# Kernel tuning notes

Hardware: AMD Instinct MI355X
Metric: run time of the kernel (lower is better)

## Reference

```python
import jax, jax.numpy as jnp
import numpy as np

B, N, M, C = 32, 4096, 512, 256  # batch, grid points, retained modes, latent channels


def setup_inputs() -> dict:
    key = jax.random.key(0)
    k1, k2 = jax.random.split(key)
    v = jax.random.normal(k1, (B, N, C), dtype=jnp.float32)
    # glorot-style scale for a (C, C) per-mode transform: std = 1/sqrt(C)
    transform_R = jax.random.normal(k2, (M, C, C), dtype=jnp.float32) * np.float32(1.0 / np.sqrt(C))
    return {"v": v, "transform_R": transform_R}


def reference(v, transform_R):
    # v: (B, N, C) real; transform_R: (M, C, C) real, applied to complex modes
    n = v.shape[1]
    m = transform_R.shape[0]
    f = jnp.fft.rfft(v, axis=1)                     # (B, N//2+1, C) complex64
    fm = f[:, :m]                                   # keep low-frequency modes (B, M, C)
    # per-mode channel mixing: out[b,m,o] = sum_i R[m,i,o] * f[b,m,i]
    gm = jnp.einsum('mio,bmi->bmo', transform_R.astype(fm.dtype), fm)
    g = jnp.zeros_like(f).at[:, :m].set(gm)         # zero-pad high modes back
    return v + jnp.fft.irfft(g, n=n, axis=1)        # residual add, (B, N, C)
```

## Files before the change

### kernel.cpp

```cpp
#include <hip/hip_runtime.h>
#include <hip/hip_fp16.h>
#include <math.h>


constexpr int BB = 32;
constexpr int CC = 256;
constexpr int MM = 512;

constexpr float PI2_4096 = 1.5339807878856412e-3f;
constexpr float PI2_512  = 1.2271846303085130e-2f;
constexpr float PI2_64   = 9.8174770424681035e-2f;
constexpr float PI_4     = 0.78539816339744831f;

typedef _Float16 f16x8 __attribute__((ext_vector_type(8)));
typedef float f32x4 __attribute__((ext_vector_type(4)));

__device__ __forceinline__ float2 cadd(float2 a, float2 b){ return make_float2(a.x+b.x, a.y+b.y); }
__device__ __forceinline__ float2 csub(float2 a, float2 b){ return make_float2(a.x-b.x, a.y-b.y); }
__device__ __forceinline__ float2 cmulf(float2 a, float2 b){ return make_float2(a.x*b.x - a.y*b.y, a.x*b.y + a.y*b.x); }

template<int S>
__device__ __forceinline__ void dif8(float2 x[8]) {
    const float R = 0.70710678118654752f;
    const float Sf = (float)S;
    float2 a0=cadd(x[0],x[4]), a1=cadd(x[1],x[5]), a2=cadd(x[2],x[6]), a3=cadd(x[3],x[7]);
    float2 d0=csub(x[0],x[4]), d1=csub(x[1],x[5]), d2=csub(x[2],x[6]), d3=csub(x[3],x[7]);
    float2 t5 = cmulf(d1, make_float2(R, -R*Sf));
    float2 t6 = make_float2(Sf*d2.y, -Sf*d2.x);
    float2 t7 = cmulf(d3, make_float2(-R, -R*Sf));
    float2 b0=cadd(a0,a2), b1=cadd(a1,a3), b2=csub(a0,a2), e3=csub(a1,a3);
    float2 b3=make_float2(Sf*e3.y, -Sf*e3.x);
    float2 b4=cadd(d0,t6), b5=cadd(t5,t7), b6=csub(d0,t6), e7=csub(t5,t7);
    float2 b7=make_float2(Sf*e7.y, -Sf*e7.x);
    x[0]=cadd(b0,b1); x[4]=csub(b0,b1);
    x[2]=cadd(b2,b3); x[6]=csub(b2,b3);
    x[1]=cadd(b4,b5); x[5]=csub(b4,b5);
    x[3]=cadd(b6,b7); x[7]=csub(b6,b7);
}

__device__ __forceinline__ void twid7(float2 x[8], float ang) {
    float s, c;
    __sincosf(ang, &s, &c);
    float2 w = make_float2(c, s), cur = w;
    x[1] = cmulf(x[1], cur);
    #pragma unroll
    for (int k = 2; k < 8; ++k) { cur = cmulf(cur, w); x[k] = cmulf(x[k], cur); }
}

__global__ __launch_bounds__(256) void k1a_kernel(const float* __restrict__ v,
                                                  __half2* __restrict__ ybuf, int b0) {
    __shared__ float2 T[64 * 33];
    const int blk = blockIdx.x;
    const int ct = blk & 1;
    const int n2 = (blk >> 1) & 63;
    const int bl = blk >> 7;
    const int bat = b0 + bl;
    const int t = threadIdx.x;
    const int p = t & 63;
    const int g = t >> 6;

    const float* vb = v + ((size_t)bat << 20) + (size_t)n2 * CC + ct * 128 + 2 * p;
    float2 X[2][8];
    #pragma unroll
    for (int s = 0; s < 2; ++s) {
        const int bd = g + 4 * s;
        #pragma unroll
        for (int a = 0; a < 8; ++a)
            X[s][a] = *(const float2*)(vb + (size_t)(8 * a + bd) * 16384);
    }
    #pragma unroll
    for (int s = 0; s < 2; ++s) {
        const int bd = g + 4 * s;
        dif8<1>(X[s]);
        twid7(X[s], -PI2_64 * (float)bd);
    }

    __half2* yb = ybuf + (size_t)bl * (64 * 64 * 128) + ct * 64 + p;
    #pragma unroll
    for (int h = 0; h < 2; ++h) {
        if (h) __syncthreads();
        {
            float2* row = T + p * 33;
            #pragma unroll
            for (int s = 0; s < 2; ++s) {
                const int bd = g + 4 * s;
                #pragma unroll
                for (int q = 0; q < 4; ++q) row[bd + 8 * q] = X[s][4 * h + q];
            }
        }
        __syncthreads();
        {
            const int k0 = g + 4 * h;
            float2 Y[8];
            const float2* row = T + p * 33 + 8 * g;
            #pragma unroll
            for (int b = 0; b < 8; ++b) Y[b] = row[b];
            dif8<1>(Y);
            float bs, bc, ss, sc;
            __sincosf(-PI2_4096 * (float)(n2 * k0), &bs, &bc);
            __sincosf(-PI2_512 * (float)n2, &ss, &sc);
            float2 cur = make_float2(bc, bs), stp = make_float2(sc, ss);
            #pragma unroll
            for (int k1b = 0; k1b < 8; ++k1b) {
                float2 r = cmulf(Y[k1b], cur);
                yb[(size_t)((k0 + 8 * k1b) * 64 + n2) * 128] = __floats2half2_rn(r.x, r.y);
                cur = cmulf(cur, stp);
            }
        }
    }
}

__global__ __launch_bounds__(256) void k1b_kernel(const __half2* __restrict__ ybuf,
                                                  __half2* __restrict__ zbuf, int b0) {
    __shared__ float2 T[64 * 33];
    const int blk = blockIdx.x;
    const int ct = blk & 1;
    const int k1 = (blk >> 1) & 63;
    const int bl = blk >> 7;
    const int bat = b0 + bl;
    const int t = threadIdx.x;
    const int p = t & 63;
    const int g = t >> 6;
    const float R = 0.70710678118654752f;

    const __half2* yb = ybuf + (size_t)bl * (64 * 64 * 128) + (size_t)k1 * (64 * 128) + ct * 64 + p;
    float2 X[2][8];
    #pragma unroll
    for (int s = 0; s < 2; ++s) {
        const int bd = g + 4 * s;
        #pragma unroll
        for (int a = 0; a < 8; ++a)
            X[s][a] = __half22float2(yb[(size_t)(8 * a + bd) * 128]);
    }
    #pragma unroll
    for (int s = 0; s < 2; ++s) {
        const int bd = g + 4 * s;
        dif8<1>(X[s]);
        twid7(X[s], -PI2_64 * (float)bd);
    }

    __half2* zb = zbuf + ((size_t)(bat * 64 + k1) * 16) * 128 + ct * 64 + p;
    #pragma unroll
    for (int h = 0; h < 2; ++h) {
        if (h) __syncthreads();
        {
            float2* row = T + p * 33;
            #pragma unroll
            for (int s = 0; s < 2; ++s) {
                const int bd = g + 4 * s;
                #pragma unroll
                for (int q = 0; q < 4; ++q) row[bd + 8 * q] = X[s][4 * h + q];
            }
        }
        __syncthreads();
        {
            const int k20 = g + 4 * h;
            float2 r[8];
            const float2* row = T + p * 33 + 8 * g;
            #pragma unroll
            for (int b = 0; b < 8; ++b) r[b] = row[b];
            float2 sum0 = make_float2(0.f, 0.f);
            #pragma unroll
            for (int b = 0; b < 8; ++b) sum0 = cadd(sum0, r[b]);
            float2 e0 = csub(r[0], r[4]);
            float2 e1 = csub(r[1], r[5]);
            float2 e2 = csub(r[2], r[6]);
            float2 e3 = csub(r[3], r[7]);
            float2 sum7 = cadd(cadd(e0, cmulf(e1, make_float2(R, R))),
                               cadd(make_float2(-e2.y, e2.x), cmulf(e3, make_float2(-R, R))));
            zb[(size_t)k20 * 128]       = __floats2half2_rn(sum0.x, sum0.y);
            zb[(size_t)(k20 + 8) * 128] = __floats2half2_rn(sum7.x, sum7.y);
        }
    }
}

__device__ __forceinline__ int swzh(int r, int col) {
    return r * 256 + (col ^ ((r & 7) << 3));
}

__global__ __launch_bounds__(256) void k2_kernel(const __half2* __restrict__ zbuf,
                                                 const float* __restrict__ R,
                                                 __half* __restrict__ gre,
                                                 __half* __restrict__ gim) {
    __shared__ __align__(16) __half XT[64 * 256];
    const int mh = blockIdx.x & 1;
    const int m  = blockIdx.x >> 1;
    const int t = threadIdx.x;
    const int k1 = m & 63, k2 = m >> 6;
    int k1p, jp;
    if (k1 == 0) { k1p = 0;       jp = (k2 == 0) ? 0 : (16 - k2); }
    else         { k1p = 64 - k1; jp = 15 - k2; }
    {
        const int b  = t & 31;
        const int pg = t >> 5;
        const __half2* zm = zbuf + ((size_t)(b * 64 + k1 ) * 16 + k2) * 128;
        const __half2* zp = zbuf + ((size_t)(b * 64 + k1p) * 16 + jp) * 128;
        #pragma unroll
        for (int q = 0; q < 16; ++q) {
            int pp = pg + 8 * q;
            float2 a = __half22float2(zm[pp]);
            float2 c = __half22float2(zp[pp]);
            *(__half2*)&XT[swzh(b,      2 * pp)] = __floats2half2_rn(0.5f * (a.x + c.x), 0.5f * (a.y + c.y));
            *(__half2*)&XT[swzh(b + 32, 2 * pp)] = __floats2half2_rn(0.5f * (a.y - c.y), 0.5f * (c.x - a.x));
        }
    }
    __syncthreads();

    const int w  = t >> 6;
    const int l  = t & 63;
    const int lr = l & 15;
    const int kg = l >> 4;
    const int colbase = mh * 128 + w * 32;

    f32x4 acc[4][2];
    #pragma unroll
    for (int mt = 0; mt < 4; ++mt)
        #pragma unroll
        for (int nt = 0; nt < 2; ++nt)
            acc[mt][nt] = (f32x4){0.f, 0.f, 0.f, 0.f};

    const float* Rb = R + (size_t)m * 65536 + colbase + lr;

    float rv[2][16];
    #pragma unroll
    for (int nt = 0; nt < 2; ++nt)
        #pragma unroll
        for (int j = 0; j < 8; ++j)
            rv[0][nt * 8 + j] = Rb[(size_t)(kg * 8 + j) * 256 + nt * 16];

    #pragma unroll
    for (int kt = 0; kt < 8; ++kt) {
        const int cur = kt & 1, nxt = cur ^ 1;
        if (kt < 7) {
            const float* rp = Rb + (size_t)((kt + 1) * 32 + kg * 8) * 256;
            #pragma unroll
            for (int nt = 0; nt < 2; ++nt)
                #pragma unroll
                for (int j = 0; j < 8; ++j)
                    rv[nxt][nt * 8 + j] = rp[(size_t)j * 256 + nt * 16];
        }
        f16x8 afrag[4];
        #pragma unroll
        for (int mt = 0; mt < 4; ++mt)
            afrag[mt] = *(const f16x8*)&XT[swzh(mt * 16 + lr, kt * 32 + kg * 8)];
        #pragma unroll
        for (int nt = 0; nt < 2; ++nt) {
            f16x8 bhi, blo;
            #pragma unroll
            for (int j = 0; j < 8; ++j) {
                float r = rv[cur][nt * 8 + j];
                _Float16 hh = (_Float16)r;
                bhi[j] = hh;
                blo[j] = (_Float16)(r - (float)hh);
            }
            #pragma unroll
            for (int mt = 0; mt < 4; ++mt) {
                acc[mt][nt] = __builtin_amdgcn_mfma_f32_16x16x32_f16(afrag[mt], bhi, acc[mt][nt], 0, 0, 0);
                acc[mt][nt] = __builtin_amdgcn_mfma_f32_16x16x32_f16(afrag[mt], blo, acc[mt][nt], 0, 0, 0);
            }
        }
    }

    #pragma unroll
    for (int mt = 0; mt < 4; ++mt) {
        __half* plane = (mt < 2) ? gre : gim;
        const int bb = (mt & 1) * 16 + kg * 4;
        #pragma unroll
        for (int nt = 0; nt < 2; ++nt) {
            const int n = colbase + nt * 16 + lr;
            #pragma unroll
            for (int j = 0; j < 4; ++j) {
                plane[((size_t)m * BB + (bb + j)) * CC + n] = __float2half_rn(acc[mt][nt][j]);
            }
        }
    }
}

__global__ __launch_bounds__(256) void k3a_kernel(const __half* __restrict__ gre,
                                                  const __half* __restrict__ gim,
                                                  __half2* __restrict__ tbuf, int b0) {
    const int blk = blockIdx.x;
    const int ct = blk & 1;
    const int k1 = (blk >> 1) & 63;
    const int bl = blk >> 7;
    const int bat = b0 + bl;
    const int t = threadIdx.x;
    const int p = t & 63;
    const int g = t >> 6;

    float2 Zd[8], Zc[8];
    #pragma unroll
    for (int k20 = 0; k20 < 8; ++k20) {
        int m = k1 + 64 * k20;
        size_t off = ((size_t)m * BB + bat) * CC + ct * 128 + 2 * p;
        float2 a = __half22float2(*(const __half2*)(gre + off));
        float2 c = __half22float2(*(const __half2*)(gim + off));
        Zd[k20] = make_float2(a.x - c.y, c.x + a.y);
        int mp = 512 - k1 - 64 * k20;
        if (mp != 512) {
            size_t offp = ((size_t)mp * BB + bat) * CC + ct * 128 + 2 * p;
            float2 ap = __half22float2(*(const __half2*)(gre + offp));
            float2 cp = __half22float2(*(const __half2*)(gim + offp));
            Zc[k20] = make_float2(ap.x + cp.y, ap.y - cp.x);
        } else {
            Zc[k20] = make_float2(0.f, 0.f);
        }
    }

    __half2* tb = tbuf + (size_t)bl * (64 * 64 * 128) + (size_t)k1 * 128 + ct * 64 + p;
    #pragma unroll
    for (int s = 0; s < 2; ++s) {
        const int bd = g + 4 * s;
        float w8s, w8c;
        __sincosf(-PI_4 * (float)bd, &w8s, &w8c);
        float2 u[8];
        #pragma unroll
        for (int k20 = 0; k20 < 8; ++k20)
            u[k20] = cadd(Zd[k20], cmulf(Zc[k20], make_float2(w8c, w8s)));
        twid7(u, PI2_64 * (float)bd);
        dif8<-1>(u);
        float bs, bc, ss, sc;
        __sincosf(PI2_4096 * (float)(bd * k1), &bs, &bc);
        __sincosf(PI2_512 * (float)k1, &ss, &sc);
        float2 cur = make_float2(bc, bs), stp = make_float2(sc, ss);
        #pragma unroll
        for (int a = 0; a < 8; ++a) {
            float2 r = cmulf(u[a], cur);
            tb[(size_t)(8 * a + bd) * (64 * 128)] = __floats2half2_rn(r.x, r.y);
            cur = cmulf(cur, stp);
        }
    }
}

__global__ __launch_bounds__(256) void k3b_kernel(const __half2* __restrict__ tbuf,
                                                  const float* __restrict__ v,
                                                  float* __restrict__ out, int b0) {
    __shared__ float2 T[64 * 33];
    const int blk = blockIdx.x;
    const int ct = blk & 1;
    const int n2 = (blk >> 1) & 63;
    const int bl = blk >> 7;
    const int bat = b0 + bl;
    const int t = threadIdx.x;
    const int p = t & 63;
    const int g = t >> 6;

    const __half2* tb = tbuf + (size_t)bl * (64 * 64 * 128) + (size_t)n2 * (64 * 128) + ct * 64 + p;
    float2 X[2][8];
    #pragma unroll
    for (int s = 0; s < 2; ++s) {
        const int be = g + 4 * s;
        #pragma unroll
        for (int a = 0; a < 8; ++a)
            X[s][a] = __half22float2(tb[(size_t)(8 * a + be) * 128]);
    }
    #pragma unroll
    for (int s = 0; s < 2; ++s) {
        const int be = g + 4 * s;
        dif8<-1>(X[s]);
        twid7(X[s], PI2_64 * (float)be);
    }

    const float sc = 1.0f / 4096.0f;
    const float* vb = v   + ((size_t)bat << 20) + (size_t)n2 * CC + ct * 128 + 2 * p;
    float*       ob = out + ((size_t)bat << 20) + (size_t)n2 * CC + ct * 128 + 2 * p;
    #pragma unroll
    for (int h = 0; h < 2; ++h) {
        if (h) __syncthreads();
        {
            float2* row = T + p * 33;
            #pragma unroll
            for (int s = 0; s < 2; ++s) {
                const int be = g + 4 * s;
                #pragma unroll
                for (int q = 0; q < 4; ++q) row[be + 8 * q] = X[s][4 * h + q];
            }
        }
        __syncthreads();
        {
            const int j0 = g + 4 * h;
            float2 r[8];
            const float2* row = T + p * 33 + 8 * g;
            #pragma unroll
            for (int b = 0; b < 8; ++b) r[b] = row[b];
            dif8<-1>(r);
            #pragma unroll
            for (int j1 = 0; j1 < 8; ++j1) {
                int n1 = j0 + 8 * j1;
                size_t off = (size_t)n1 * 16384;
                float2 vz = *(const float2*)(vb + off);
                float2 o = make_float2(vz.x + r[j1].x * sc, vz.y + r[j1].y * sc);
                *(float2*)(ob + off) = o;
            }
        }
    }
}

extern "C" void kernel_launch(void* const* d_in, const int* in_sizes, int n_in,
                              void* d_out, int out_size, void* d_ws, size_t ws_size,
                              hipStream_t stream) {
    const float* v = (const float*)d_in[0];
    const float* R = (const float*)d_in[1];
    float* out = (float*)d_out;

    __half2* ybuf = (__half2*)d_ws;
    __half2* zbuf = ybuf + (size_t)16 * 64 * 64 * 128;
    __half*  gre  = (__half*)(zbuf + (size_t)32 * 64 * 16 * 128);
    __half*  gim  = gre + (size_t)MM * BB * CC;

    for (int h = 0; h < 2; ++h) {
        k1a_kernel<<<2048, 256, 0, stream>>>(v, ybuf, h * 16);
        k1b_kernel<<<2048, 256, 0, stream>>>(ybuf, zbuf, h * 16);
    }
    k2_kernel<<<1024, 256, 0, stream>>>(zbuf, R, gre, gim);
    for (int h = 0; h < 2; ++h) {
        k3a_kernel<<<2048, 256, 0, stream>>>(gre, gim, ybuf, h * 16);
        k3b_kernel<<<2048, 256, 0, stream>>>(ybuf, v, out, h * 16);
    }
}
```

Baseline: 432.0 us.

## Fuse forward FFT stages into one kernel with shared-memory transpose

Replaces the two-pass forward FFT (k1a writes an fp16 intermediate buffer to global memory, k1b reads it back) with a single kernel that keeps the intermediate in LDS. Each block handles one batch and a 16-channel slice for all 4096 points, doing the first two radix-8 stages in registers and the last stage from swizzled shared memory. Lane pairs combine partial sums with shuffles. This removes a global round trip and two launches, at the cost of heavy register use (64 float2 per thread plus 32 held halves) and only 512 blocks, so occupancy may drop.

New measurement: 473.6 us. 1.1x slower.

```diff
diff --git a/kernel.cpp b/kernel.cpp
--- a/kernel.cpp
+++ b/kernel.cpp
@@ -47,129 +47,113 @@
     for (int k = 2; k < 8; ++k) { cur = cmulf(cur, w); x[k] = cmulf(x[k], cur); }
 }
 
-__global__ __launch_bounds__(256) void k1a_kernel(const float* __restrict__ v,
-                                                  __half2* __restrict__ ybuf, int b0) {
-    __shared__ float2 T[64 * 33];
+__device__ __forceinline__ int k1f_sidx(int k1r, int n2, int chp) {
+    return (k1r * 64 + (n2 ^ (k1r & 3))) * 8 + chp;
+}
+
+__global__ __launch_bounds__(512, 2) void k1f_kernel(const float* __restrict__ v,
+                                                     __half2* __restrict__ zbuf) {
+    __shared__ __half2 S[32 * 64 * 8];
     const int blk = blockIdx.x;
-    const int ct = blk & 1;
-    const int n2 = (blk >> 1) & 63;
-    const int bl = blk >> 7;
-    const int bat = b0 + bl;
+    const int cg  = blk & 15;
+    const int bat = blk >> 4;
     const int t = threadIdx.x;
-    const int p = t & 63;
-    const int g = t >> 6;
-
-    const float* vb = v + ((size_t)bat << 20) + (size_t)n2 * CC + ct * 128 + 2 * p;
-    float2 X[2][8];
-    #pragma unroll
-    for (int s = 0; s < 2; ++s) {
-        const int bd = g + 4 * s;
-        #pragma unroll
-        for (int a = 0; a < 8; ++a)
-            X[s][a] = *(const float2*)(vb + (size_t)(8 * a + bd) * 16384);
-    }
-    #pragma unroll
-    for (int s = 0; s < 2; ++s) {
-        const int bd = g + 4 * s;
-        dif8<1>(X[s]);
-        twid7(X[s], -PI2_64 * (float)bd);
-    }
-
-    __half2* yb = ybuf + (size_t)bl * (64 * 64 * 128) + ct * 64 + p;
+    const int chp = t & 7;
+    const int n2  = t >> 3;
+
+    const float* vb = v + ((size_t)bat << 20) + (size_t)n2 * CC + 16 * cg + 2 * chp;
+    float2 X[8][8];
+    #pragma unroll
+    for (int be = 0; be < 8; ++be)
+        #pragma unroll
+        for (int al = 0; al < 8; ++al)
+            X[be][al] = *(const float2*)(vb + (size_t)(8 * al + be) * 16384);
+
+    #pragma unroll
+    for (int be = 0; be < 8; ++be) {
+        dif8<1>(X[be]);
+        twid7(X[be], -PI2_64 * (float)be);
+    }
+
+    float s1, c1, s8, c8;
+    __sincosf(-PI2_4096 * (float)n2, &s1, &c1);
+    __sincosf(-PI2_512  * (float)n2, &s8, &c8);
+    const float2 w1 = make_float2(c1, s1);
+    const float2 w8 = make_float2(c8, s8);
+
+    __half2 held[32];
+    float2 base = make_float2(1.f, 0.f);
+    #pragma unroll
+    for (int k0 = 0; k0 < 8; ++k0) {
+        float2 Y[8];
+        #pragma unroll
+        for (int b = 0; b < 8; ++b) Y[b] = X[b][k0];
+        dif8<1>(Y);
+        float2 cur = base;
+        #pragma unroll
+        for (int k1b = 0; k1b < 8; ++k1b) {
+            float2 r = cmulf(Y[k1b], cur);
+            __half2 hh = __floats2half2_rn(r.x, r.y);
+            if (k1b < 4) S[k1f_sidx(k0 + 8 * k1b, n2, chp)] = hh;
+            else         held[k0 + 8 * (k1b - 4)] = hh;
+            cur = cmulf(cur, w8);
+        }
+        base = cmulf(base, w1);
+    }
+    __syncthreads();
+
+    const int sub  = t & 1;
+    const int task = t >> 1;
+    const int chB  = task & 7;
+    const int k1r  = task >> 3;
+    const int cpg  = 8 * cg + chB;
+    const float Rc = 0.70710678118654752f;
+    const float2 w7tab[4] = { make_float2(1.f, 0.f), make_float2(Rc, Rc),
+                              make_float2(0.f, 1.f), make_float2(-Rc, Rc) };
+    const float sg = sub ? -1.f : 1.f;
+
     #pragma unroll
     for (int h = 0; h < 2; ++h) {
-        if (h) __syncthreads();
-        {
-            float2* row = T + p * 33;
-            #pragma unroll
-            for (int s = 0; s < 2; ++s) {
-                const int bd = g + 4 * s;
-                #pragma unroll
-                for (int q = 0; q < 4; ++q) row[bd + 8 * q] = X[s][4 * h + q];
-            }
-        }
-        __syncthreads();
-        {
-            const int k0 = g + 4 * h;
-            float2 Y[8];
-            const float2* row = T + p * 33 + 8 * g;
-            #pragma unroll
-            for (int b = 0; b < 8; ++b) Y[b] = row[b];
-            dif8<1>(Y);
-            float bs, bc, ss, sc;
-            __sincosf(-PI2_4096 * (float)(n2 * k0), &bs, &bc);
-            __sincosf(-PI2_512 * (float)n2, &ss, &sc);
-            float2 cur = make_float2(bc, bs), stp = make_float2(sc, ss);
-            #pragma unroll
-            for (int k1b = 0; k1b < 8; ++k1b) {
-                float2 r = cmulf(Y[k1b], cur);
-                yb[(size_t)((k0 + 8 * k1b) * 64 + n2) * 128] = __floats2half2_rn(r.x, r.y);
-                cur = cmulf(cur, stp);
-            }
-        }
-    }
-}
-
-__global__ __launch_bounds__(256) void k1b_kernel(const __half2* __restrict__ ybuf,
-                                                  __half2* __restrict__ zbuf, int b0) {
-    __shared__ float2 T[64 * 33];
-    const int blk = blockIdx.x;
-    const int ct = blk & 1;
-    const int k1 = (blk >> 1) & 63;
-    const int bl = blk >> 7;
-    const int bat = b0 + bl;
-    const int t = threadIdx.x;
-    const int p = t & 63;
-    const int g = t >> 6;
-    const float R = 0.70710678118654752f;
-
-    const __half2* yb = ybuf + (size_t)bl * (64 * 64 * 128) + (size_t)k1 * (64 * 128) + ct * 64 + p;
-    float2 X[2][8];
-    #pragma unroll
-    for (int s = 0; s < 2; ++s) {
-        const int bd = g + 4 * s;
-        #pragma unroll
-        for (int a = 0; a < 8; ++a)
-            X[s][a] = __half22float2(yb[(size_t)(8 * a + bd) * 128]);
-    }
-    #pragma unroll
-    for (int s = 0; s < 2; ++s) {
-        const int bd = g + 4 * s;
-        dif8<1>(X[s]);
-        twid7(X[s], -PI2_64 * (float)bd);
-    }
-
-    __half2* zb = zbuf + ((size_t)(bat * 64 + k1) * 16) * 128 + ct * 64 + p;
-    #pragma unroll
-    for (int h = 0; h < 2; ++h) {
-        if (h) __syncthreads();
-        {
-            float2* row = T + p * 33;
-            #pragma unroll
-            for (int s = 0; s < 2; ++s) {
-                const int bd = g + 4 * s;
-                #pragma unroll
-                for (int q = 0; q < 4; ++q) row[bd + 8 * q] = X[s][4 * h + q];
-            }
-        }
-        __syncthreads();
-        {
-            const int k20 = g + 4 * h;
-            float2 r[8];
-            const float2* row = T + p * 33 + 8 * g;
-            #pragma unroll
-            for (int b = 0; b < 8; ++b) r[b] = row[b];
-            float2 sum0 = make_float2(0.f, 0.f);
-            #pragma unroll
-            for (int b = 0; b < 8; ++b) sum0 = cadd(sum0, r[b]);
-            float2 e0 = csub(r[0], r[4]);
-            float2 e1 = csub(r[1], r[5]);
-            float2 e2 = csub(r[2], r[6]);
-            float2 e3 = csub(r[3], r[7]);
-            float2 sum7 = cadd(cadd(e0, cmulf(e1, make_float2(R, R))),
-                               cadd(make_float2(-e2.y, e2.x), cmulf(e3, make_float2(-R, R))));
-            zb[(size_t)k20 * 128]       = __floats2half2_rn(sum0.x, sum0.y);
-            zb[(size_t)(k20 + 8) * 128] = __floats2half2_rn(sum7.x, sum7.y);
+        if (h) {
+            __syncthreads();
+            #pragma unroll
+            for (int i = 0; i < 32; ++i) S[k1f_sidx(i, n2, chp)] = held[i];
+            __syncthreads();
+        }
+        const int k1 = k1r + 32 * h;
+
+        float2 p0[8], p7[8];
+        #pragma unroll
+        for (int k = 0; k < 8; ++k) { p0[k] = make_float2(0.f, 0.f); p7[k] = make_float2(0.f, 0.f); }
+
+        #pragma unroll
+        for (int di = 0; di < 4; ++di) {
+            const int delta = 4 * sub + di;
+            float2 y[8];
+            #pragma unroll
+            for (int gm = 0; gm < 8; ++gm)
+                y[gm] = __half22float2(S[k1f_sidx(k1r, 8 * gm + delta, chB)]);
+            dif8<1>(y);
+            twid7(y, -PI2_64 * (float)delta);
+            const float2 w7s = make_float2(sg * w7tab[di].x, sg * w7tab[di].y);
+            #pragma unroll
+            for (int k20 = 0; k20 < 8; ++k20) {
+                p0[k20] = cadd(p0[k20], y[k20]);
+                p7[k20] = cadd(p7[k20], cmulf(y[k20], w7s));
+            }
+        }
+        #pragma unroll
+        for (int k20 = 0; k20 < 8; ++k20) {
+            p0[k20].x += __shfl_xor(p0[k20].x, 1);
+            p0[k20].y += __shfl_xor(p0[k20].y, 1);
+            p7[k20].x += __shfl_xor(p7[k20].x, 1);
+            p7[k20].y += __shfl_xor(p7[k20].y, 1);
+        }
+        __half2* zb = zbuf + ((size_t)(bat * 64 + k1) * 16 + 8 * sub) * 128 + cpg;
+        #pragma unroll
+        for (int k20 = 0; k20 < 8; ++k20) {
+            float2 vz = sub ? p7[k20] : p0[k20];
+            zb[(size_t)k20 * 128] = __floats2half2_rn(vz.x, vz.y);
         }
     }
 }
@@ -403,18 +387,15 @@
     const float* R = (const float*)d_in[1];
     float* out = (float*)d_out;
 
-    __half2* ybuf = (__half2*)d_ws;
-    __half2* zbuf = ybuf + (size_t)16 * 64 * 64 * 128;
+    __half2* tbuf = (__half2*)d_ws;
+    __half2* zbuf = tbuf + (size_t)16 * 64 * 64 * 128;
     __half*  gre  = (__half*)(zbuf + (size_t)32 * 64 * 16 * 128);
     __half*  gim  = gre + (size_t)MM * BB * CC;
 
-    for (int h = 0; h < 2; ++h) {
-        k1a_kernel<<<2048, 256, 0, stream>>>(v, ybuf, h * 16);
-        k1b_kernel<<<2048, 256, 0, stream>>>(ybuf, zbuf, h * 16);
-    }
+    k1f_kernel<<<512, 512, 0, stream>>>(v, zbuf);
     k2_kernel<<<1024, 256, 0, stream>>>(zbuf, R, gre, gim);
     for (int h = 0; h < 2; ++h) {
-        k3a_kernel<<<2048, 256, 0, stream>>>(gre, gim, ybuf, h * 16);
-        k3b_kernel<<<2048, 256, 0, stream>>>(ybuf, v, out, h * 16);
-    }
-}
+        k3a_kernel<<<2048, 256, 0, stream>>>(gre, gim, tbuf, h * 16);
+        k3b_kernel<<<2048, 256, 0, stream>>>(tbuf, v, out, h * 16);
+    }
+}
```
